# Performance work log

Measured on AMD Instinct MI355X. Metric: run time of the kernel, lower is better.

## Reference

```python
import jax, jax.numpy as jnp
import numpy as np

B, S, H = 2, 2048, 1024
E, I, K = 8, 4096, 2


def setup_inputs() -> dict:
    key = jax.random.key(0)
    ks = jax.random.split(key, 5)
    scale_h = 1.0 / np.sqrt(H)
    scale_i = 1.0 / np.sqrt(I)
    x = jax.random.normal(ks[0], (B, S, H), dtype=jnp.float32)
    gate_w = jax.random.normal(ks[1], (E, H), dtype=jnp.float32) * scale_h   # router Linear weight [out=E, in=H]
    wg = jax.random.normal(ks[2], (E, I, H), dtype=jnp.float32) * scale_h    # gate_proj weights, stacked over experts
    wu = jax.random.normal(ks[3], (E, I, H), dtype=jnp.float32) * scale_h    # up_proj weights
    wd = jax.random.normal(ks[4], (E, H, I), dtype=jnp.float32) * scale_i    # down_proj weights
    return {"x": x, "gate_w": gate_w, "wg": wg, "wu": wu, "wd": wd}


def _moe_forward(x, gate_w, wg, wu, wd):
    b, s, h = x.shape
    x_flat = x.reshape(-1, h)                       # [T, H]
    logits = x_flat @ gate_w.T                      # [T, E]
    top_v, top_i = jax.lax.top_k(logits, K)         # [T, K]
    probs = jax.nn.softmax(top_v.astype(jnp.float32), axis=-1).astype(logits.dtype)  # [T, K]
    # per-token combine weight for each expert: sum_k probs[:,k] * 1[top_i[:,k]==e]
    one_hot = jax.nn.one_hot(top_i, E, dtype=probs.dtype)   # [T, K, E]
    combine = jnp.einsum('tk,tke->et', probs, one_hot)       # [E, T]
    # loop over experts via scan: acc += w_e * SwiGLU_e(x)
    def body(acc, ws):
        wge, wue, wde, we = ws
        hidden = jax.nn.silu(x_flat @ wge.T) * (x_flat @ wue.T)  # [T, I]
        return acc + we[:, None] * (hidden @ wde.T), None
    out, _ = jax.lax.scan(body, jnp.zeros_like(x_flat), (wg, wu, wd, combine))
    return out.reshape(b, s, h)


def reference(x, gate_w, wg, wu, wd):
    return _moe_forward(x, gate_w, wg, wu, wd)
```

## Files before the change

kernel.cpp:

```cpp
#include <hip/hip_runtime.h>
#include <math.h>

#define T_TOK 4096
#define H_DIM 1024
#define E_NUM 8
#define I_DIM 4096

typedef __attribute__((ext_vector_type(4))) float f32x4;
typedef __attribute__((ext_vector_type(8))) short bf16x8;

__device__ inline unsigned short f2bf(float f) {
  unsigned int u = __float_as_uint(f);
  u += 0x7fffu + ((u >> 16) & 1u);
  return (unsigned short)(u >> 16);
}

__device__ inline void cvt_store4(unsigned short* dst, const float* src) {
  f32x4 v = *reinterpret_cast<const f32x4*>(src);
  ushort4 o;
  o.x = f2bf(v[0]); o.y = f2bf(v[1]); o.z = f2bf(v[2]); o.w = f2bf(v[3]);
  *reinterpret_cast<ushort4*>(dst) = o;
}

__device__ inline void gll16(const void* g, void* l) {
  __builtin_amdgcn_global_load_lds(
      (const __attribute__((address_space(1))) void*)g,
      (__attribute__((address_space(3))) void*)l, 16, 0, 0);
}

__global__ __launch_bounds__(64) void k_router(const float* __restrict__ x,
                                               const float* __restrict__ gw,
                                               unsigned short* __restrict__ xb,
                                               int2* __restrict__ tokE,
                                               float2* __restrict__ tokP,
                                               int* __restrict__ counts) {
  const int t = blockIdx.x;
  const int l = threadIdx.x;
  const float* xr = x + (size_t)t * H_DIM;
  unsigned short* xbr = xb ? xb + (size_t)t * H_DIM : nullptr;
  float acc[E_NUM];
#pragma unroll
  for (int e = 0; e < E_NUM; e++) acc[e] = 0.f;
  for (int h = l; h < H_DIM; h += 64) {
    float xv = xr[h];
    if (xbr) xbr[h] = f2bf(xv);
#pragma unroll
    for (int e = 0; e < E_NUM; e++) acc[e] += xv * gw[e * H_DIM + h];
  }
#pragma unroll
  for (int e = 0; e < E_NUM; e++) {
#pragma unroll
    for (int off = 32; off > 0; off >>= 1) acc[e] += __shfl_xor(acc[e], off);
  }
  if (l == 0) {
    float v0 = -1e30f, v1 = -1e30f;
    int e0 = 0, e1 = 0;
#pragma unroll
    for (int e = 0; e < E_NUM; e++) {
      float v = acc[e];
      if (v > v0) { v1 = v0; e1 = e0; v0 = v; e0 = e; }
      else if (v > v1) { v1 = v; e1 = e; }
    }
    float ex = expf(v1 - v0);
    float p0 = 1.f / (1.f + ex);
    float p1 = ex * p0;
    tokE[t] = make_int2(e0, e1);
    tokP[t] = make_float2(p0, p1);
    atomicAdd(&counts[e0], 1);
    atomicAdd(&counts[e1], 1);
  }
}

__global__ void k_offsets(const int* __restrict__ counts, int* __restrict__ offsets) {
  if (threadIdx.x == 0 && blockIdx.x == 0) {
    int s = 0;
    for (int e = 0; e < E_NUM; e++) { offsets[e] = s; s += counts[e]; }
    offsets[E_NUM] = s;
  }
}

__global__ __launch_bounds__(256) void k_scatter(const int2* __restrict__ tokE,
                                                 const float2* __restrict__ tokP,
                                                 const int* __restrict__ counts,
                                                 int* __restrict__ cursor,
                                                 int* __restrict__ slot_tok,
                                                 float* __restrict__ slot_w,
                                                 int* __restrict__ inv_slot) {
  int t = blockIdx.x * 256 + threadIdx.x;
  if (t >= T_TOK) return;
  int offs[E_NUM];
  int s = 0;
#pragma unroll
  for (int e = 0; e < E_NUM; e++) { offs[e] = s; s += counts[e]; }
  int2 e = tokE[t];
  float2 p = tokP[t];
  int pos0 = atomicAdd(&cursor[e.x], 1);
  int s0 = offs[e.x] + pos0;
  slot_tok[s0] = t;
  slot_w[s0] = p.x;
  inv_slot[2 * t] = s0;
  int pos1 = atomicAdd(&cursor[e.y], 1);
  int s1 = offs[e.y] + pos1;
  slot_tok[s1] = t;
  slot_w[s1] = p.y;
  inv_slot[2 * t + 1] = s1;
}

__global__ __launch_bounds__(256) void k_cvt(const float* __restrict__ src,
                                             unsigned short* __restrict__ dst,
                                             int n4) {
  int i = blockIdx.x * 256 + threadIdx.x;
  const int stride = gridDim.x * 256;
  for (; i < n4; i += stride) {
    f32x4 v = reinterpret_cast<const f32x4*>(src)[i];
    ushort4 o;
    o.x = f2bf(v[0]); o.y = f2bf(v[1]); o.z = f2bf(v[2]); o.w = f2bf(v[3]);
    reinterpret_cast<ushort4*>(dst)[i] = o;
  }
}

__global__ __launch_bounds__(256) void k_cvt2(const float* __restrict__ srcA,
                                              unsigned short* __restrict__ dstA,
                                              const float* __restrict__ srcB,
                                              unsigned short* __restrict__ dstB,
                                              int n4) {
  int i = blockIdx.x * 256 + threadIdx.x;
  const int stride = gridDim.x * 256;
  for (; i < 2 * n4; i += stride) {
    const float* s = (i < n4) ? srcA : srcB;
    unsigned short* d = (i < n4) ? dstA : dstB;
    int j = (i < n4) ? i : i - n4;
    f32x4 v = reinterpret_cast<const f32x4*>(s)[j];
    ushort4 o;
    o.x = f2bf(v[0]); o.y = f2bf(v[1]); o.z = f2bf(v[2]); o.w = f2bf(v[3]);
    reinterpret_cast<ushort4*>(d)[j] = o;
  }
}

__device__ inline int expert_base(const int* counts, int e) {
  int s = 0;
  for (int i = 0; i < e; i++) s += counts[i];
  return s;
}

__global__ __launch_bounds__(256, 2) void k_gateup2(
    const unsigned short* __restrict__ xb, const unsigned short* __restrict__ wgb,
    const unsigned short* __restrict__ wub, const int* __restrict__ counts,
    const int* __restrict__ slot_tok, unsigned short* __restrict__ hidden) {
  const int e = blockIdx.z;
  const int cnt = counts[e];
  const int m0 = blockIdx.y * 128;
  if (m0 >= cnt) return;
  const int n0 = blockIdx.x * 128;
  const int base = expert_base(counts, e);

  __shared__ unsigned short As[128 * 64];
  __shared__ unsigned short Bg[128 * 64];
  __shared__ unsigned short Bu[128 * 64];

  const int tid = threadIdx.x;
  const int wave = tid >> 6;
  const int lane = tid & 63;
  const int wm = (wave >> 1) * 64;
  const int wn = (wave & 1) * 64;
  const int lr = lane & 15;
  const int lk = lane >> 4;

  const int sr = lane >> 3;
  const int sc = lane & 7;
  const int swz = ((sc ^ sr) << 3);

  const size_t wbase = (size_t)e * I_DIM * H_DIM;
  const unsigned short* srcA[4];
  const unsigned short* srcBg[4];
  const unsigned short* srcBu[4];
  unsigned short* dstA[4];
  unsigned short* dstBg[4];
  unsigned short* dstBu[4];
#pragma unroll
  for (int i = 0; i < 4; i++) {
    int row = wave * 32 + i * 8 + sr;
    int gr = m0 + row; if (gr > cnt - 1) gr = cnt - 1;
    srcA[i]  = xb + (size_t)slot_tok[base + gr] * H_DIM + swz;
    srcBg[i] = wgb + wbase + (size_t)(n0 + row) * H_DIM + swz;
    srcBu[i] = wub + wbase + (size_t)(n0 + row) * H_DIM + swz;
    dstA[i]  = &As[(wave * 32 + i * 8) * 64];
    dstBg[i] = &Bg[(wave * 32 + i * 8) * 64];
    dstBu[i] = &Bu[(wave * 32 + i * 8) * 64];
  }

  f32x4 accg[4][4], accu[4][4];
#pragma unroll
  for (int i = 0; i < 4; i++)
#pragma unroll
    for (int j = 0; j < 4; j++) {
      accg[i][j] = (f32x4){0.f, 0.f, 0.f, 0.f};
      accu[i][j] = (f32x4){0.f, 0.f, 0.f, 0.f};
    }

  const int xorr = ((lr & 7) << 3);

  for (int k0 = 0; k0 < H_DIM; k0 += 64) {
#pragma unroll
    for (int i = 0; i < 4; i++) {
      gll16(srcA[i] + k0, dstA[i]);
      gll16(srcBg[i] + k0, dstBg[i]);
      gll16(srcBu[i] + k0, dstBu[i]);
    }
    __syncthreads();
#pragma unroll
    for (int kh = 0; kh < 2; kh++) {
      const int koff = (((kh * 4 + lk) << 3) ^ xorr);
      bf16x8 af[4];
#pragma unroll
      for (int mf = 0; mf < 4; mf++)
        af[mf] = *reinterpret_cast<const bf16x8*>(&As[(wm + mf * 16 + lr) * 64 + koff]);
#pragma unroll
      for (int nf = 0; nf < 4; nf++) {
        const int roff = (wn + nf * 16 + lr) * 64 + koff;
        bf16x8 bg = *reinterpret_cast<const bf16x8*>(&Bg[roff]);
        bf16x8 bu = *reinterpret_cast<const bf16x8*>(&Bu[roff]);
#pragma unroll
        for (int mf = 0; mf < 4; mf++) {
          accg[mf][nf] = __builtin_amdgcn_mfma_f32_16x16x32_bf16(af[mf], bg, accg[mf][nf], 0, 0, 0);
          accu[mf][nf] = __builtin_amdgcn_mfma_f32_16x16x32_bf16(af[mf], bu, accu[mf][nf], 0, 0, 0);
        }
      }
    }
    __syncthreads();
  }

#pragma unroll
  for (int mf = 0; mf < 4; mf++) {
#pragma unroll
    for (int j = 0; j < 4; j++) {
      int row = wm + mf * 16 + lk * 4 + j;
      if (m0 + row < cnt) {
        size_t hbase = (size_t)(base + m0 + row) * I_DIM;
#pragma unroll
        for (int nf = 0; nf < 4; nf++) {
          int col = n0 + wn + nf * 16 + lr;
          float g = accg[mf][nf][j];
          float u = accu[mf][nf][j];
          float h = g / (1.f + expf(-g)) * u;
          hidden[hbase + col] = f2bf(h);
        }
      }
    }
  }
}

__global__ __launch_bounds__(256, 2) void k_down7(
    const unsigned short* __restrict__ hidden, const unsigned short* __restrict__ wdb,
    const int* __restrict__ counts, const int* __restrict__ slot_tok,
    const float* __restrict__ slot_w, float* __restrict__ part) {
  const int e = blockIdx.z;
  const int cnt = counts[e];
  const int m0 = blockIdx.y * 128;
  if (m0 >= cnt) return;
  const int n0 = blockIdx.x * 128;
  const int base = expert_base(counts, e);

  __shared__ unsigned short As[128 * 64];
  __shared__ unsigned short Bs[128 * 64];

  const int tid = threadIdx.x;
  const int wave = tid >> 6;
  const int lane = tid & 63;
  const int wm = (wave >> 1) * 64;
  const int wn = (wave & 1) * 64;
  const int lr = lane & 15;
  const int lk = lane >> 4;

  const int sr = lane >> 3;
  const int sc = lane & 7;
  const int swz = ((sc ^ sr) << 3);

  const unsigned short* srcA[4];
  const unsigned short* srcB[4];
  unsigned short* dstA[4];
  unsigned short* dstB[4];
#pragma unroll
  for (int i = 0; i < 4; i++) {
    int row = wave * 32 + i * 8 + sr;
    int gr = m0 + row; if (gr > cnt - 1) gr = cnt - 1;
    srcA[i] = hidden + (size_t)(base + gr) * I_DIM + swz;
    srcB[i] = wdb + (size_t)e * H_DIM * I_DIM + (size_t)(n0 + row) * I_DIM + swz;
    dstA[i] = &As[(wave * 32 + i * 8) * 64];
    dstB[i] = &Bs[(wave * 32 + i * 8) * 64];
  }

  f32x4 acc[4][4];
#pragma unroll
  for (int i = 0; i < 4; i++)
#pragma unroll
    for (int j = 0; j < 4; j++) acc[i][j] = (f32x4){0.f, 0.f, 0.f, 0.f};

  const int xorr = ((lr & 7) << 3);

  for (int k0 = 0; k0 < I_DIM; k0 += 64) {
#pragma unroll
    for (int i = 0; i < 4; i++) {
      gll16(srcA[i] + k0, dstA[i]);
      gll16(srcB[i] + k0, dstB[i]);
    }
    __syncthreads();
#pragma unroll
    for (int kh = 0; kh < 2; kh++) {
      const int koff = (((kh * 4 + lk) << 3) ^ xorr);
      bf16x8 af[4];
#pragma unroll
      for (int mf = 0; mf < 4; mf++)
        af[mf] = *reinterpret_cast<const bf16x8*>(&As[(wm + mf * 16 + lr) * 64 + koff]);
#pragma unroll
      for (int nf = 0; nf < 4; nf++) {
        bf16x8 bf = *reinterpret_cast<const bf16x8*>(&Bs[(wn + nf * 16 + lr) * 64 + koff]);
#pragma unroll
        for (int mf = 0; mf < 4; mf++)
          acc[mf][nf] = __builtin_amdgcn_mfma_f32_16x16x32_bf16(af[mf], bf, acc[mf][nf], 0, 0, 0);
      }
    }
    __syncthreads();
  }

#pragma unroll
  for (int mf = 0; mf < 4; mf++) {
#pragma unroll
    for (int j = 0; j < 4; j++) {
      int row = wm + mf * 16 + lk * 4 + j;
      if (m0 + row < cnt) {
        int slot = base + m0 + row;
        float w = slot_w[slot];
        float* prow = part + (size_t)slot * H_DIM;
#pragma unroll
        for (int nf = 0; nf < 4; nf++) {
          int col = n0 + wn + nf * 16 + lr;
          prow[col] = w * acc[mf][nf][j];
        }
      }
    }
  }
}

__global__ __launch_bounds__(256) void k_gather(const float* __restrict__ part,
                                                const int* __restrict__ inv_slot,
                                                float* __restrict__ out) {
  int i = blockIdx.x * 256 + threadIdx.x;
  const int n4 = T_TOK * H_DIM / 4;
  if (i >= n4) return;
  const int perrow = H_DIM / 4;
  int t = i / perrow;
  int c = i - t * perrow;
  int s0 = inv_slot[2 * t];
  int s1 = inv_slot[2 * t + 1];
  f32x4 a = reinterpret_cast<const f32x4*>(part)[(size_t)s0 * perrow + c];
  f32x4 b = reinterpret_cast<const f32x4*>(part)[(size_t)s1 * perrow + c];
  reinterpret_cast<f32x4*>(out)[i] = a + b;
}

__global__ __launch_bounds__(256) void k_gateup_v1(
    const float* __restrict__ x, const float* __restrict__ wg,
    const float* __restrict__ wu, const int* __restrict__ counts,
    const int* __restrict__ offsets, const int* __restrict__ slot_tok,
    unsigned short* __restrict__ hidden) {
  const int e = blockIdx.z;
  const int cnt = counts[e];
  const int m0 = blockIdx.y * 128;
  if (m0 >= cnt) return;
  const int n0 = blockIdx.x * 128;
  const int base = offsets[e];

  __shared__ unsigned short As[128 * 40];
  __shared__ unsigned short Bgs[128 * 40];
  __shared__ unsigned short Bus[128 * 40];

  const int tid = threadIdx.x;
  const int wave = tid >> 6;
  const int lane = tid & 63;
  const int wm = (wave >> 1) * 64;
  const int wn = (wave & 1) * 64;
  const int lr = lane & 15;
  const int lk = lane >> 4;
  const int r_sub = tid >> 3;
  const int kq = (tid & 7) * 4;

  const float* wge = wg + (size_t)e * I_DIM * H_DIM;
  const float* wue = wu + (size_t)e * I_DIM * H_DIM;

  const float* aptr[4];
  const float* bgptr[4];
  const float* buptr[4];
#pragma unroll
  for (int p = 0; p < 4; p++) {
    int row = p * 32 + r_sub;
    int gr = m0 + row;
    if (gr > cnt - 1) gr = cnt - 1;
    aptr[p] = x + (size_t)slot_tok[base + gr] * H_DIM + kq;
    bgptr[p] = wge + (size_t)(n0 + row) * H_DIM + kq;
    buptr[p] = wue + (size_t)(n0 + row) * H_DIM + kq;
  }

  f32x4 accg[4][4], accu[4][4];
#pragma unroll
  for (int i = 0; i < 4; i++)
#pragma unroll
    for (int j = 0; j < 4; j++) {
      accg[i][j] = (f32x4){0.f, 0.f, 0.f, 0.f};
      accu[i][j] = (f32x4){0.f, 0.f, 0.f, 0.f};
    }

  for (int k0 = 0; k0 < H_DIM; k0 += 32) {
#pragma unroll
    for (int p = 0; p < 4; p++) {
      int row = p * 32 + r_sub;
      cvt_store4(&As[row * 40 + kq], aptr[p] + k0);
      cvt_store4(&Bgs[row * 40 + kq], bgptr[p] + k0);
      cvt_store4(&Bus[row * 40 + kq], buptr[p] + k0);
    }
    __syncthreads();
    bf16x8 af[4];
#pragma unroll
    for (int mf = 0; mf < 4; mf++)
      af[mf] = *reinterpret_cast<const bf16x8*>(&As[(wm + mf * 16 + lr) * 40 + lk * 8]);
#pragma unroll
    for (int nf = 0; nf < 4; nf++) {
      bf16x8 bg = *reinterpret_cast<const bf16x8*>(&Bgs[(wn + nf * 16 + lr) * 40 + lk * 8]);
      bf16x8 bu = *reinterpret_cast<const bf16x8*>(&Bus[(wn + nf * 16 + lr) * 40 + lk * 8]);
#pragma unroll
      for (int mf = 0; mf < 4; mf++) {
        accg[mf][nf] = __builtin_amdgcn_mfma_f32_16x16x32_bf16(af[mf], bg, accg[mf][nf], 0, 0, 0);
        accu[mf][nf] = __builtin_amdgcn_mfma_f32_16x16x32_bf16(af[mf], bu, accu[mf][nf], 0, 0, 0);
      }
    }
    __syncthreads();
  }

#pragma unroll
  for (int mf = 0; mf < 4; mf++) {
#pragma unroll
    for (int j = 0; j < 4; j++) {
      int row = wm + mf * 16 + lk * 4 + j;
      if (m0 + row < cnt) {
        size_t hbase = (size_t)(base + m0 + row) * I_DIM;
#pragma unroll
        for (int nf = 0; nf < 4; nf++) {
          int col = n0 + wn + nf * 16 + lr;
          float g = accg[mf][nf][j];
          float u = accu[mf][nf][j];
          float h = g / (1.f + expf(-g)) * u;
          hidden[hbase + col] = f2bf(h);
        }
      }
    }
  }
}

__global__ __launch_bounds__(256) void k_down_v1(
    const unsigned short* __restrict__ hidden, const float* __restrict__ wd,
    const int* __restrict__ counts, const int* __restrict__ offsets,
    const int* __restrict__ slot_tok, const float* __restrict__ slot_w,
    float* __restrict__ out) {
  const int e = blockIdx.z;
  const int cnt = counts[e];
  const int m0 = blockIdx.y * 128;
  if (m0 >= cnt) return;
  const int n0 = blockIdx.x * 128;
  const int base = offsets[e];

  __shared__ unsigned short As[128 * 40];
  __shared__ unsigned short Bs[128 * 40];

  const int tid = threadIdx.x;
  const int wave = tid >> 6;
  const int lane = tid & 63;
  const int wm = (wave >> 1) * 64;
  const int wn = (wave & 1) * 64;
  const int lr = lane & 15;
  const int lk = lane >> 4;
  const int r_sub = tid >> 3;
  const int kq = (tid & 7) * 4;

  const unsigned short* ap[4];
  const float* bp[4];
#pragma unroll
  for (int p = 0; p < 4; p++) {
    int row = p * 32 + r_sub;
    int gr = m0 + row;
    if (gr > cnt - 1) gr = cnt - 1;
    ap[p] = hidden + (size_t)(base + gr) * I_DIM + kq;
    bp[p] = wd + (size_t)e * H_DIM * I_DIM + (size_t)(n0 + row) * I_DIM + kq;
  }

  f32x4 acc[4][4];
#pragma unroll
  for (int i = 0; i < 4; i++)
#pragma unroll
    for (int j = 0; j < 4; j++) acc[i][j] = (f32x4){0.f, 0.f, 0.f, 0.f};

  for (int k0 = 0; k0 < I_DIM; k0 += 32) {
#pragma unroll
    for (int p = 0; p < 4; p++) {
      int row = p * 32 + r_sub;
      *reinterpret_cast<ushort4*>(&As[row * 40 + kq]) =
          *reinterpret_cast<const ushort4*>(ap[p] + k0);
      cvt_store4(&Bs[row * 40 + kq], bp[p] + k0);
    }
    __syncthreads();
    bf16x8 af[4];
#pragma unroll
    for (int mf = 0; mf < 4; mf++)
      af[mf] = *reinterpret_cast<const bf16x8*>(&As[(wm + mf * 16 + lr) * 40 + lk * 8]);
#pragma unroll
    for (int nf = 0; nf < 4; nf++) {
      bf16x8 bf = *reinterpret_cast<const bf16x8*>(&Bs[(wn + nf * 16 + lr) * 40 + lk * 8]);
#pragma unroll
      for (int mf = 0; mf < 4; mf++)
        acc[mf][nf] = __builtin_amdgcn_mfma_f32_16x16x32_bf16(af[mf], bf, acc[mf][nf], 0, 0, 0);
    }
    __syncthreads();
  }

#pragma unroll
  for (int mf = 0; mf < 4; mf++) {
#pragma unroll
    for (int j = 0; j < 4; j++) {
      int row = wm + mf * 16 + lk * 4 + j;
      if (m0 + row < cnt) {
        int slot = base + m0 + row;
        int t = slot_tok[slot];
        float w = slot_w[slot];
#pragma unroll
        for (int nf = 0; nf < 4; nf++) {
          int col = n0 + wn + nf * 16 + lr;
          atomicAdd(&out[(size_t)t * H_DIM + col], w * acc[mf][nf][j]);
        }
      }
    }
  }
}

extern "C" void kernel_launch(void* const* d_in, const int* in_sizes, int n_in,
                              void* d_out, int out_size, void* d_ws, size_t ws_size,
                              hipStream_t stream) {
  const float* x = (const float*)d_in[0];
  const float* gate_w = (const float*)d_in[1];
  const float* wg = (const float*)d_in[2];
  const float* wu = (const float*)d_in[3];
  const float* wd = (const float*)d_in[4];
  float* out = (float*)d_out;

  char* ws = (char*)d_ws;
  int* counts = (int*)(ws + 0);
  int* cursor = (int*)(ws + 64);
  int* offsets = (int*)(ws + 128);
  int2* tokE = (int2*)(ws + 256);
  float2* tokP = (float2*)(ws + 256 + 32768);
  int* slot_tok = (int*)(ws + 256 + 65536);
  float* slot_w = (float*)(ws + 256 + 98304);
  int* inv_slot = (int*)(ws + 256 + 131072);

  const size_t OFF_XB  = 262144;
  const size_t OFF_HID = OFF_XB + 8388608;
  const size_t OFF_WG  = OFF_HID + 67108864;
  const size_t OFF_WU  = OFF_WG + 67108864;
  const size_t NEED    = OFF_WU + 67108864;

  const bool fast = (ws_size >= NEED);
  unsigned short* xb = fast ? (unsigned short*)(ws + OFF_XB) : nullptr;

  hipMemsetAsync(d_ws, 0, 256, stream);

  k_router<<<T_TOK, 64, 0, stream>>>(x, gate_w, xb, tokE, tokP, counts);
  k_scatter<<<T_TOK / 256, 256, 0, stream>>>(tokE, tokP, counts, cursor,
                                             slot_tok, slot_w, inv_slot);

  if (fast) {
    unsigned short* hid = (unsigned short*)(ws + OFF_HID);
    unsigned short* wgb = (unsigned short*)(ws + OFF_WG);
    unsigned short* wub = (unsigned short*)(ws + OFF_WU);
    unsigned short* wdb = wgb;
    float* part = (float*)(ws + OFF_WU);

    k_cvt2<<<4096, 256, 0, stream>>>(wg, wgb, wu, wub, E_NUM * I_DIM * H_DIM / 4);
    k_gateup2<<<dim3(I_DIM / 128, 32, E_NUM), 256, 0, stream>>>(
        xb, wgb, wub, counts, slot_tok, hid);
    k_cvt<<<2048, 256, 0, stream>>>(wd, wdb, E_NUM * H_DIM * I_DIM / 4);
    k_down7<<<dim3(H_DIM / 128, 32, E_NUM), 256, 0, stream>>>(
        hid, wdb, counts, slot_tok, slot_w, part);
    k_gather<<<T_TOK * H_DIM / 4 / 256, 256, 0, stream>>>(part, inv_slot, out);
  } else {
    unsigned short* hid = (unsigned short*)(ws + 131328 + 32768);
    hipMemsetAsync(d_out, 0, (size_t)T_TOK * H_DIM * sizeof(float), stream);
    k_offsets<<<1, 64, 0, stream>>>(counts, offsets);
    k_gateup_v1<<<dim3(I_DIM / 128, 32, E_NUM), 256, 0, stream>>>(
        x, wg, wu, counts, offsets, slot_tok, hid);
    k_down_v1<<<dim3(H_DIM / 128, 32, E_NUM), 256, 0, stream>>>(
        hid, wd, counts, offsets, slot_tok, slot_w, out);
  }
}
```

Before: 566.3 us.

## Double-buffer gate/up GEMM with 256-row tiles and 512-thread blocks

Replaces the gate/up expert GEMM with a version using 256x128 tiles, 8 waves per block, and double-buffered LDS with async global-to-LDS loads issued two K-steps ahead. Uses explicit vmcnt waits, raw barriers and s_setprio around the MFMA block so loads for the next tile overlap compute. The larger M tile improves weight reuse per token row, but can waste work for experts with small token counts. LDS use grows to 128 KB per block, which may cut occupancy.

```diff
diff --git a/kernel.cpp b/kernel.cpp
--- a/kernel.cpp
+++ b/kernel.cpp
@@ -143,107 +143,132 @@
   return s;
 }
 
-__global__ __launch_bounds__(256, 2) void k_gateup2(
+__global__ __launch_bounds__(512, 2) void k_gateup9(
     const unsigned short* __restrict__ xb, const unsigned short* __restrict__ wgb,
     const unsigned short* __restrict__ wub, const int* __restrict__ counts,
     const int* __restrict__ slot_tok, unsigned short* __restrict__ hidden) {
   const int e = blockIdx.z;
   const int cnt = counts[e];
-  const int m0 = blockIdx.y * 128;
+  const int m0 = blockIdx.y * 256;
   if (m0 >= cnt) return;
   const int n0 = blockIdx.x * 128;
   const int base = expert_base(counts, e);
 
-  __shared__ unsigned short As[128 * 64];
-  __shared__ unsigned short Bg[128 * 64];
-  __shared__ unsigned short Bu[128 * 64];
+  __shared__ unsigned short As[2][256 * 64];
+  __shared__ unsigned short Bg[2][128 * 64];
+  __shared__ unsigned short Bu[2][128 * 64];
 
   const int tid = threadIdx.x;
   const int wave = tid >> 6;
   const int lane = tid & 63;
-  const int wm = (wave >> 1) * 64;
-  const int wn = (wave & 1) * 64;
+  const int wm = (wave >> 2) * 128;
+  const int wn = (wave & 3) * 32;
   const int lr = lane & 15;
   const int lk = lane >> 4;
 
-  const int sr = lane >> 3;
-  const int sc = lane & 7;
-  const int swz = ((sc ^ sr) << 3);
-
-  const size_t wbase = (size_t)e * I_DIM * H_DIM;
-  const unsigned short* srcA[4];
-  const unsigned short* srcBg[4];
-  const unsigned short* srcBu[4];
-  unsigned short* dstA[4];
-  unsigned short* dstBg[4];
-  unsigned short* dstBu[4];
+  const int srow = lane >> 3;
+  const int schk = lane & 7;
+  const int swz = ((schk ^ srow) << 3);
+  const int ldsw = wave * 8 * 64;
+
+  const size_t wboff = (size_t)e * (size_t)I_DIM * H_DIM;
+  const unsigned short* pA[4];
+  const unsigned short* pBg[2];
+  const unsigned short* pBu[2];
 #pragma unroll
   for (int i = 0; i < 4; i++) {
-    int row = wave * 32 + i * 8 + sr;
-    int gr = m0 + row; if (gr > cnt - 1) gr = cnt - 1;
-    srcA[i]  = xb + (size_t)slot_tok[base + gr] * H_DIM + swz;
-    srcBg[i] = wgb + wbase + (size_t)(n0 + row) * H_DIM + swz;
-    srcBu[i] = wub + wbase + (size_t)(n0 + row) * H_DIM + swz;
-    dstA[i]  = &As[(wave * 32 + i * 8) * 64];
-    dstBg[i] = &Bg[(wave * 32 + i * 8) * 64];
-    dstBu[i] = &Bu[(wave * 32 + i * 8) * 64];
-  }
-
-  f32x4 accg[4][4], accu[4][4];
-#pragma unroll
-  for (int i = 0; i < 4; i++)
-#pragma unroll
-    for (int j = 0; j < 4; j++) {
+    int r = i * 64 + wave * 8 + srow;
+    int gr = m0 + r; if (gr > cnt - 1) gr = cnt - 1;
+    pA[i] = xb + (size_t)slot_tok[base + gr] * H_DIM + swz;
+  }
+#pragma unroll
+  for (int i = 0; i < 2; i++) {
+    int r = i * 64 + wave * 8 + srow;
+    pBg[i] = wgb + wboff + (size_t)(n0 + r) * H_DIM + swz;
+    pBu[i] = wub + wboff + (size_t)(n0 + r) * H_DIM + swz;
+  }
+
+  f32x4 accg[8][2], accu[8][2];
+#pragma unroll
+  for (int i = 0; i < 8; i++)
+#pragma unroll
+    for (int j = 0; j < 2; j++) {
       accg[i][j] = (f32x4){0.f, 0.f, 0.f, 0.f};
       accu[i][j] = (f32x4){0.f, 0.f, 0.f, 0.f};
     }
 
-  const int xorr = ((lr & 7) << 3);
-
-  for (int k0 = 0; k0 < H_DIM; k0 += 64) {
-#pragma unroll
-    for (int i = 0; i < 4; i++) {
-      gll16(srcA[i] + k0, dstA[i]);
-      gll16(srcBg[i] + k0, dstBg[i]);
-      gll16(srcBu[i] + k0, dstBu[i]);
-    }
-    __syncthreads();
-#pragma unroll
-    for (int kh = 0; kh < 2; kh++) {
-      const int koff = (((kh * 4 + lk) << 3) ^ xorr);
-      bf16x8 af[4];
-#pragma unroll
-      for (int mf = 0; mf < 4; mf++)
-        af[mf] = *reinterpret_cast<const bf16x8*>(&As[(wm + mf * 16 + lr) * 64 + koff]);
-#pragma unroll
-      for (int nf = 0; nf < 4; nf++) {
-        const int roff = (wn + nf * 16 + lr) * 64 + koff;
-        bf16x8 bg = *reinterpret_cast<const bf16x8*>(&Bg[roff]);
-        bf16x8 bu = *reinterpret_cast<const bf16x8*>(&Bu[roff]);
-#pragma unroll
-        for (int mf = 0; mf < 4; mf++) {
-          accg[mf][nf] = __builtin_amdgcn_mfma_f32_16x16x32_bf16(af[mf], bg, accg[mf][nf], 0, 0, 0);
-          accu[mf][nf] = __builtin_amdgcn_mfma_f32_16x16x32_bf16(af[mf], bu, accu[mf][nf], 0, 0, 0);
-        }
+  const int ar = (wm + lr) * 64;
+  const int br = (wn + lr) * 64;
+  const int xr = lr & 7;
+  const int c0 = ((lk ^ xr) << 3);
+  const int c1 = (((4 + lk) ^ xr) << 3);
+
+#define GU9_ISSUE(B, K)                                   \
+  do {                                                    \
+    gll16(pBg[0] + (K), &Bg[B][0 * 4096 + ldsw]);         \
+    gll16(pBg[1] + (K), &Bg[B][1 * 4096 + ldsw]);         \
+    gll16(pBu[0] + (K), &Bu[B][0 * 4096 + ldsw]);         \
+    gll16(pBu[1] + (K), &Bu[B][1 * 4096 + ldsw]);         \
+    gll16(pA[0] + (K), &As[B][0 * 4096 + ldsw]);          \
+    gll16(pA[1] + (K), &As[B][1 * 4096 + ldsw]);          \
+    gll16(pA[2] + (K), &As[B][2 * 4096 + ldsw]);          \
+    gll16(pA[3] + (K), &As[B][3 * 4096 + ldsw]);          \
+  } while (0)
+
+  asm volatile("s_waitcnt vmcnt(0)" ::: "memory");
+
+  GU9_ISSUE(0, 0);
+  GU9_ISSUE(1, 64);
+
+  const int NT = H_DIM / 64;
+  for (int t = 0; t < NT; t++) {
+    const int cur = t & 1;
+    asm volatile("s_waitcnt vmcnt(8)" ::: "memory");
+    __builtin_amdgcn_s_barrier();
+
+    bf16x8 fg[2][2], fu[2][2];
+#pragma unroll
+    for (int nf = 0; nf < 2; nf++) {
+      fg[nf][0] = *(const bf16x8*)&Bg[cur][br + nf * 1024 + c0];
+      fg[nf][1] = *(const bf16x8*)&Bg[cur][br + nf * 1024 + c1];
+      fu[nf][0] = *(const bf16x8*)&Bu[cur][br + nf * 1024 + c0];
+      fu[nf][1] = *(const bf16x8*)&Bu[cur][br + nf * 1024 + c1];
+    }
+    __builtin_amdgcn_s_setprio(1);
+#pragma unroll
+    for (int mf = 0; mf < 8; mf++) {
+      bf16x8 a0 = *(const bf16x8*)&As[cur][ar + mf * 1024 + c0];
+      bf16x8 a1 = *(const bf16x8*)&As[cur][ar + mf * 1024 + c1];
+#pragma unroll
+      for (int nf = 0; nf < 2; nf++) {
+        accg[mf][nf] = __builtin_amdgcn_mfma_f32_16x16x32_bf16(a0, fg[nf][0], accg[mf][nf], 0, 0, 0);
+        accg[mf][nf] = __builtin_amdgcn_mfma_f32_16x16x32_bf16(a1, fg[nf][1], accg[mf][nf], 0, 0, 0);
+        accu[mf][nf] = __builtin_amdgcn_mfma_f32_16x16x32_bf16(a0, fu[nf][0], accu[mf][nf], 0, 0, 0);
+        accu[mf][nf] = __builtin_amdgcn_mfma_f32_16x16x32_bf16(a1, fu[nf][1], accu[mf][nf], 0, 0, 0);
       }
     }
-    __syncthreads();
-  }
-
-#pragma unroll
-  for (int mf = 0; mf < 4; mf++) {
+    __builtin_amdgcn_s_setprio(0);
+    __builtin_amdgcn_s_barrier();
+
+    const int kn = (t + 2 < NT) ? (t + 2) * 64 : 0;
+    GU9_ISSUE(cur, kn);
+  }
+#undef GU9_ISSUE
+  asm volatile("s_waitcnt vmcnt(0)" ::: "memory");
+
+#pragma unroll
+  for (int mf = 0; mf < 8; mf++) {
 #pragma unroll
     for (int j = 0; j < 4; j++) {
       int row = wm + mf * 16 + lk * 4 + j;
       if (m0 + row < cnt) {
         size_t hbase = (size_t)(base + m0 + row) * I_DIM;
 #pragma unroll
-        for (int nf = 0; nf < 4; nf++) {
+        for (int nf = 0; nf < 2; nf++) {
           int col = n0 + wn + nf * 16 + lr;
           float g = accg[mf][nf][j];
           float u = accu[mf][nf][j];
-          float h = g / (1.f + expf(-g)) * u;
-          hidden[hbase + col] = f2bf(h);
+          hidden[hbase + col] = f2bf(g / (1.f + expf(-g)) * u);
         }
       }
     }
@@ -582,7 +607,7 @@
     float* part = (float*)(ws + OFF_WU);
 
     k_cvt2<<<4096, 256, 0, stream>>>(wg, wgb, wu, wub, E_NUM * I_DIM * H_DIM / 4);
-    k_gateup2<<<dim3(I_DIM / 128, 32, E_NUM), 256, 0, stream>>>(
+    k_gateup9<<<dim3(I_DIM / 128, 16, E_NUM), 512, 0, stream>>>(
         xb, wgb, wub, counts, slot_tok, hid);
     k_cvt<<<2048, 256, 0, stream>>>(wd, wdb, E_NUM * H_DIM * I_DIM / 4);
     k_down7<<<dim3(H_DIM / 128, 32, E_NUM), 256, 0, stream>>>(
```

After: 604.1 us. 1.07x slower.
